# Optimization experiments

Measured on AMD Instinct MI355X. Metric: run time of the kernel, lower is better.

## Reference

```python
import jax, jax.numpy as jnp
import numpy as np

MAX_FREQ = 10
CORR_RADIUS = 2
PATCH = 9


def _gelu(x):
    return jax.nn.gelu(x, approximate=False)


def _project(coords, R, C0, f, pp):
    # coords [N,3] -> uv [ncams,N,2], cam-space z [ncams,N]
    d = coords[None, :, :] - C0[:, None, :]
    Xc = jnp.einsum('cij,cnj->cni', R, d)
    z = jnp.maximum(Xc[..., 2:3], 1e-6)
    uv = Xc[..., :2] / z * f[:, None, :] + pp[:, None, :]
    return uv, Xc[..., 2]


def _fourier(x, max_freq):
    freqs = (2.0 ** jnp.arange(max_freq, dtype=x.dtype)) * jnp.pi
    xf = x[..., None] * freqs
    enc = jnp.concatenate([jnp.sin(xf), jnp.cos(xf)], axis=-1)  # [...,D,2F]
    return enc.reshape(enc.shape[:-2] + (x.shape[-1] * 2 * max_freq,))


def _bilinear_time(img, t, gx, gy):
    # img [B,T,C,H,W]; t [B,K] int; gx,gy [B,K,P] normalized grid in [-1,1]
    # grid_sample(align_corners=False, padding_mode='zeros') via direct 4-tap gather
    B, T, C, H, W = img.shape
    x = (gx + 1.0) * 0.5 * W - 0.5
    y = (gy + 1.0) * 0.5 * H - 0.5
    x0 = jnp.floor(x)
    y0 = jnp.floor(y)
    wx = (x - x0)[..., None]
    wy = (y - y0)[..., None]
    x0 = x0.astype(jnp.int32)
    y0 = y0.astype(jnp.int32)
    b = jnp.arange(B)[:, None, None]
    tt = t[:, :, None]

    def tap(yy, xx):
        ok = ((xx >= 0) & (xx < W) & (yy >= 0) & (yy < H))[..., None]
        v = img[b, tt, :, jnp.clip(yy, 0, H - 1), jnp.clip(xx, 0, W - 1)]  # [B,K,P,C]
        return v * ok.astype(v.dtype)

    return (tap(y0, x0) * (1 - wx) * (1 - wy) + tap(y0, x0 + 1) * wx * (1 - wy)
            + tap(y0 + 1, x0) * (1 - wx) * wy + tap(y0 + 1, x0 + 1) * wx * wy)


def _conv2d(x, w, b):
    y = jax.lax.conv_general_dilated(x, w, (1, 1), 'SAME', dimension_numbers=('NCHW', 'OIHW', 'NCHW'))
    return y + b[None, :, None, None]


def _conv3d(x, w, b):
    y = jax.lax.conv_general_dilated(x, w, (1, 1, 1), 'SAME', dimension_numbers=('NCDHW', 'OIDHW', 'NCDHW'))
    return y + b[None, :, None, None, None]


def reference(views, cam_R, cam_center, cam_focal, cam_pp, query_coords, query_time, target_time, cube_scale, v2v_w, v2v_b, lin_vol_w, lin_vol_b, lin_pos_w, lin_pos_b, lin_depth_w, lin_depth_b, conv1_w, conv1_b, conv2_w, conv2_b, conv3_w, conv3_b, mlp1_w, mlp1_b, mlp2_w, mlp2_b, tq_emb, tt_emb, vis_emb_tab, depth_norm_scale, gate_w, gate_b, fus1_w, fus1_b, fus2_w, fus2_b):
    ncams, B, T, C, H, W = views.shape
    K = query_coords.shape[1]
    sizes = jnp.asarray([W, H], dtype=query_coords.dtype)

    # project query points to all cameras
    qflat = query_coords.reshape(-1, 3)
    p2d_flat, zc = _project(qflat, cam_R, cam_center, cam_focal, cam_pp)  # [ncams,BK,2]
    p2d_full = p2d_flat.reshape(ncams, B, K, 2)

    # fourier position embedding
    pp_n = jnp.transpose(p2d_full, (1, 2, 0, 3)) / sizes  # [B,K,ncams,2]
    embed_pos = _fourier(pp_n, MAX_FREQ) @ lin_pos_w.T + lin_pos_b

    # volume embedding: masked multi-camera cube sampling + 3D conv
    cs = 2 * CORR_RADIUS + 1
    P3 = cs ** 3
    row = (jnp.arange(cs, dtype=query_coords.dtype) - CORR_RADIUS) * (cube_scale * 2.0)
    gx3, gy3, gz3 = jnp.meshgrid(row, row, row, indexing='ij')
    xyz = jnp.stack([gx3, gy3, gz3], axis=-1).reshape(-1, 3)  # [P3,3], x outermost
    cube = (query_coords[:, :, None, :] + xyz).reshape(-1, 3)
    pc, _ = _project(cube, cam_R, cam_center, cam_focal, cam_pp)
    pc = pc.reshape(ncams, B, K, P3, 2)
    smps, msks = [], []
    for c in range(ncams):
        g = 2.0 * pc[c] / sizes - 1.0
        m = (g[..., 0] >= -1) & (g[..., 0] <= 1) & (g[..., 1] >= -1) & (g[..., 1] <= 1)
        s = _bilinear_time(views[c], query_time, g[..., 0], g[..., 1])  # [B,K,P3,C]
        smps.append(s)
        msks.append(m)
    vol = jnp.stack(smps)  # [ncams,B,K,P3,C]
    mf = jnp.stack(msks).astype(vol.dtype)[..., None]
    cnt = jnp.maximum(mf.sum(0), 1.0)
    mv = (vol * mf).sum(0) / cnt  # [B,K,P3,C]
    mv = mv.reshape(B, K, cs, cs, cs, C)  # (x,y,z,C)
    mv = jnp.transpose(mv, (0, 1, 5, 4, 3, 2)).reshape(B * K, C, cs, cs, cs)  # [(BK),C,z,y,x]
    mv = _gelu(_conv3d(mv, v2v_w, v2v_b))  # EmbedV2V: Conv3d(3,vdim,3) + GELU
    vd = mv.shape[1]
    mv = mv.reshape(B, K, vd, cs, cs, cs)
    mv = jnp.transpose(mv, (0, 1, 2, 5, 4, 3)).reshape(B, K, vd * P3)  # 'b t 1 (d total)'
    embed_volume = mv @ lin_vol_w.T + lin_vol_b
    embed_volume = jnp.broadcast_to(embed_volume[:, :, None, :], (B, K, ncams, embed_volume.shape[-1]))

    # patch embedding per camera
    lin = jnp.arange(PATCH, dtype=query_coords.dtype)
    gyy, gxx = jnp.meshgrid(lin, lin, indexing='ij')
    offs = jnp.stack([gxx - (PATCH - 1) / 2.0, gyy - (PATCH - 1) / 2.0], axis=-1)  # [P,P,2]
    pats = []
    for c in range(ncams):
        px = p2d_full[c][:, :, None, None, :] + offs  # [B,K,P,P,2]
        g = ((2.0 * px + 1.0) / sizes - 1.0).reshape(B, K, PATCH * PATCH, 2)
        s = _bilinear_time(views[c], query_time, g[..., 0], g[..., 1])  # [B,K,PP,C]
        pats.append(jnp.transpose(s.reshape(B, K, PATCH, PATCH, C), (0, 1, 4, 2, 3)))
    patches = jnp.stack(pats).reshape(ncams * B * K, C, PATCH, PATCH)
    x = _gelu(_conv2d(patches, conv1_w, conv1_b))
    x = _gelu(_conv2d(x, conv2_w, conv2_b))
    x = _gelu(_conv2d(x, conv3_w, conv3_b))
    x = x.reshape(x.shape[0], -1)  # 'b c p q -> b (c p q)'
    x = _gelu(x @ mlp1_w.T + mlp1_b)  # dropout is eval-mode identity
    emb_p = x @ mlp2_w.T + mlp2_b
    embed_patch = jnp.transpose(emb_p.reshape(ncams, B, K, -1), (1, 2, 0, 3))

    E = tq_emb.shape[1]
    embed_qt = jnp.broadcast_to(tq_emb[query_time][:, :, None, :], (B, K, ncams, E))
    embed_tt = jnp.broadcast_to(tt_emb[target_time][:, :, None, :], (B, K, ncams, E))

    # visibility (pinhole in-bounds check with margin=2)
    u = p2d_flat[..., 0]
    v = p2d_flat[..., 1]
    margin = 2.0
    vis = (zc > 0) & (u >= margin) & (u <= W - margin) & (v >= margin) & (v <= H - margin)
    vis = jnp.transpose(vis.reshape(ncams, B, K), (1, 2, 0))  # [B,K,ncams]
    embed_vis = vis_emb_tab[vis.astype(jnp.int32)]

    depths = jnp.linalg.norm(query_coords[:, :, None, :] - cam_center, axis=-1) / (cube_scale * depth_norm_scale[0])
    embed_depth = _fourier(depths[..., None], MAX_FREQ) @ lin_depth_w.T + lin_depth_b

    # gated fusion of 7 terms + fusion MLP
    terms = [embed_pos, embed_volume, embed_patch, embed_qt, embed_tt, embed_vis, embed_depth]
    gates = jax.nn.sigmoid(jnp.concatenate(terms, axis=-1) @ gate_w.T + gate_b)  # [B,K,ncams,7]
    fused = sum(gates[..., i:i + 1] * terms[i] for i in range(len(terms)))
    h = _gelu(fused @ fus1_w.T + fus1_b)
    embed_total = h @ fus2_w.T + fus2_b  # [B,K,ncams,decoder_dim]
    return embed_total, vis


def setup_inputs():
    ks = jax.random.split(jax.random.key(0), 24)
    ncams, B, T, C, H, W = 4, 2, 16, 3, 256, 256
    K, E, MF, cs, P, vdim = 256, 256, 10, 5, 9, 8
    views = jax.random.normal(ks[0], (ncams, B, T, C, H, W), jnp.float32)
    cam_R = jnp.tile(jnp.eye(3, dtype=jnp.float32)[None], (ncams, 1, 1))
    cam_center = jnp.stack([jnp.linspace(-0.5, 0.5, ncams), jnp.linspace(0.5, -0.5, ncams), jnp.full((ncams,), -5.0)], axis=-1).astype(jnp.float32)
    cam_focal = jnp.full((ncams, 2), 200.0, jnp.float32)
    cam_pp = jnp.full((ncams, 2), 128.0, jnp.float32)
    query_coords = jax.random.uniform(ks[1], (B, K, 3), jnp.float32, -1.0, 1.0)
    query_time = jax.random.randint(ks[2], (B, K), 0, T).astype(jnp.int32)
    target_time = jax.random.randint(ks[3], (B, K), 0, T).astype(jnp.int32)
    cube_scale = jnp.float32(0.02)

    def w(k, shape, s=0.02):
        return jax.random.normal(k, shape, jnp.float32) * s

    z = lambda n: jnp.zeros((n,), jnp.float32)
    return dict(
        views=views, cam_R=cam_R, cam_center=cam_center, cam_focal=cam_focal, cam_pp=cam_pp,
        query_coords=query_coords, query_time=query_time, target_time=target_time, cube_scale=cube_scale,
        v2v_w=w(ks[4], (vdim, C, 3, 3, 3)), v2v_b=z(vdim),
        lin_vol_w=w(ks[5], (E, cs ** 3 * vdim)), lin_vol_b=z(E),
        lin_pos_w=w(ks[6], (E, 4 * MF)), lin_pos_b=z(E),
        lin_depth_w=w(ks[7], (E, 2 * MF)), lin_depth_b=z(E),
        conv1_w=w(ks[8], (32, 3, 3, 3)), conv1_b=z(32),
        conv2_w=w(ks[9], (64, 32, 3, 3)), conv2_b=z(64),
        conv3_w=w(ks[10], (128, 64, 3, 3)), conv3_b=z(128),
        mlp1_w=w(ks[11], (2 * E, 128 * P * P)), mlp1_b=z(2 * E),
        mlp2_w=w(ks[12], (E, 2 * E)), mlp2_b=z(E),
        tq_emb=w(ks[13], (T, E), 1.0), tt_emb=w(ks[14], (T, E), 1.0),
        vis_emb_tab=w(ks[15], (2, E), 1.0),
        depth_norm_scale=jnp.array([500.0], jnp.float32),
        gate_w=w(ks[16], (7, 7 * E), 0.01), gate_b=z(7),
        fus1_w=w(ks[17], (4 * E, E)), fus1_b=z(4 * E),
        fus2_w=w(ks[18], (E, 4 * E)), fus2_b=z(E),
    )
```

## Files before the change

### kernel.cpp

```cpp
#include <hip/hip_runtime.h>
#include <hip/hip_bf16.h>

typedef __hip_bfloat16 bf16;
typedef __attribute__((ext_vector_type(8))) short short8;
typedef __attribute__((ext_vector_type(4))) float floatx4;

#define NC 4
#define BB 2
#define TS 16
#define CHN 3
#define HH 256
#define WW 256
#define KQ 256
#define EE 256
#define BKT 512
#define HW 65536
#define NSEG 25
#define CH1 32
#define CH1P 40
#define CH2 64
#define CH2P 72
#define PW 11

#define PB_WCL   32
#define PB_W23   160
#define PB_AUXW  416
#define PB_PROJ  424
#define PB_CUBE  936
#define PB_M1W   1448
#define PB_END   1452

__device__ __forceinline__ float tof(bf16 x){ return __bfloat162float(x); }
__device__ __forceinline__ bf16 tobf(float x){ return __float2bfloat16(x); }
__device__ __forceinline__ float gelu_f(float x){
    float t = fabsf(x) * 0.70710678118654752f;
    float k = __builtin_amdgcn_rcpf(fmaf(0.3275911f, t, 1.f));
    float p = fmaf(fmaf(fmaf(fmaf(1.061405429f, k, -1.453152027f), k,
                   1.421413741f), k, -0.284496736f), k, 0.254829592f) * k;
    float e = __expf(-t*t);
    float er = fmaf(-p, e, 1.f);
    float s = copysignf(er, x);
    return 0.5f*x*(1.f + s);
}
__device__ __forceinline__ float ldx(const void* p, size_t i, int bf){
    return bf ? tof(((const bf16*)p)[i]) : ((const float*)p)[i];
}
__device__ __forceinline__ void gload_lds16(const void* g, void* l){
    __builtin_amdgcn_global_load_lds((const __attribute__((address_space(1))) void*)g,
                                     (__attribute__((address_space(3))) void*)l, 16, 0, 0);
}
__device__ __forceinline__ unsigned pack2(float a, float b){
    union{ bf16 h[2]; unsigned u; } pk; pk.h[0]=tobf(a); pk.h[1]=tobf(b); return pk.u;
}

struct CvtArgs { const void* src[NSEG]; int dstoff[NSEG]; int cnt[NSEG]; };

struct PrepArgs {
    const void *camF, *camR, *camC, *camP, *qc, *csc;
    const void *c2w, *c3w, *linv, *f1w, *f2w, *m2w, *m1w, *views;
    const void *v2vw, *v2vb;
    const void *linpw, *lindw;
    const int* qtime;
    bf16 *w2cl, *w3cl, *linv_bf, *f1w_bf, *f2w_bf, *m2w_bf, *m1w_bf;
    float *p2d, *visf;
    float *linpwT, *lindwT;
    bf16* volf;
    void* dout;
    int* flagp;
};

union PrepSm {
    struct { float vol[3][7][7][7]; float ws[648]; float bs[8]; } cube;
    bf16 lin[10368];
};

__global__ __launch_bounds__(256) void prep_kernel(CvtArgs ca, float* __restrict__ pool, PrepArgs a)
{
    int bid = blockIdx.x, tid = threadIdx.x;
    int bf = (((const unsigned short*)a.camF)[0] != 0) ? 1 : 0;
    __shared__ PrepSm sm;

    if (bid < PB_WCL){
        for (int s=0; s<NSEG; ++s){
            const void* src = ca.src[s];
            float* d = pool + ca.dstoff[s];
            int n = ca.cnt[s];
            for (int i = bid*256 + tid; i < n; i += PB_WCL*256) d[i] = ldx(src, i, bf);
        }
    } else if (bid < PB_W23){
        int i0 = (bid-PB_WCL)*256 + tid;
        const int stride = (PB_W23-PB_WCL)*256;
        for (int i=i0; i<64*32*9; i+=stride){
            int oc=i/(32*9), r=i%(32*9), ic=r/9, tap=r%9;
            a.w2cl[tap*(64*CH1) + oc*CH1 + ic] = tobf(ldx(a.c2w, i, bf));
        }
        for (int i=i0; i<128*64*9; i+=stride){
            int oc=i/(64*9), r=i%(64*9), ic=r/9, tap=r%9;
            a.w3cl[tap*(128*CH2) + oc*CH2 + ic] = tobf(ldx(a.c3w, i, bf));
        }
    } else if (bid < PB_AUXW){
        int sub = (bid-PB_W23)>>6;
        int i0 = ((bid-PB_W23)&63)*256 + tid;
        const int stride = 64*256;
        if (sub==0){
            for (int i=i0; i<256*1024; i+=stride){
                int r=i>>10, c=i&1023;
                a.linv_bf[i] = tobf(c<1000 ? ldx(a.linv, (size_t)r*1000+c, bf) : 0.f);
            }
        } else if (sub==1){
            for (int i=i0; i<1024*256; i+=stride) a.f1w_bf[i]=tobf(ldx(a.f1w,i,bf));
        } else if (sub==2){
            for (int i=i0; i<256*1024; i+=stride) a.f2w_bf[i]=tobf(ldx(a.f2w,i,bf));
        } else {
            for (int i=i0; i<256*512; i+=stride) a.m2w_bf[i]=tobf(ldx(a.m2w,i,bf));
        }
    } else if (bid < PB_PROJ){
        if (bid==PB_AUXW && tid==0) *a.flagp = bf;
        int idx = (bid-PB_AUXW)*256 + tid;
        if (idx < NC*BKT){
            int c = idx / BKT, bk = idx % BKT;
            float dx = ldx(a.qc,bk*3+0,bf) - ldx(a.camC,c*3+0,bf);
            float dy = ldx(a.qc,bk*3+1,bf) - ldx(a.camC,c*3+1,bf);
            float dz = ldx(a.qc,bk*3+2,bf) - ldx(a.camC,c*3+2,bf);
            float X0 = ldx(a.camR,c*9+0,bf)*dx + ldx(a.camR,c*9+1,bf)*dy + ldx(a.camR,c*9+2,bf)*dz;
            float X1 = ldx(a.camR,c*9+3,bf)*dx + ldx(a.camR,c*9+4,bf)*dy + ldx(a.camR,c*9+5,bf)*dz;
            float X2 = ldx(a.camR,c*9+6,bf)*dx + ldx(a.camR,c*9+7,bf)*dy + ldx(a.camR,c*9+8,bf)*dz;
            float z = fmaxf(X2, 1e-6f);
            float u = X0/z*ldx(a.camF,c*2+0,bf) + ldx(a.camP,c*2+0,bf);
            float v = X1/z*ldx(a.camF,c*2+1,bf) + ldx(a.camP,c*2+1,bf);
            a.p2d[idx*2+0] = u; a.p2d[idx*2+1] = v;
            bool vis = (X2 > 0.f) && (u >= 2.f) && (u <= (float)WW-2.f) && (v >= 2.f) && (v <= (float)HH-2.f);
            a.visf[idx] = vis ? 1.f : 0.f;
            float vv = vis ? 1.f : 0.f;
            size_t vidx = (size_t)BB*KQ*NC*EE + (size_t)bk*NC + c;
            if (bf) ((bf16*)a.dout)[vidx] = tobf(vv);
            else    ((float*)a.dout)[vidx] = vv;
        }
    } else if (bid < PB_CUBE){
        int bk = bid - PB_PROJ;
        int c = tid & 3;
        int pg = tid >> 2;
        int b = bk >> 8;
        for (int i=tid; i<3*343; i+=256) ((float*)sm.cube.vol)[i]=0.f;
        for (int i=tid; i<648; i+=256) sm.cube.ws[i]=ldx(a.v2vw,i,bf);
        if (tid<8) sm.cube.bs[tid]=ldx(a.v2vb,tid,bf);
        __syncthreads();
        float cs2 = ldx(a.csc,0,bf) * 2.f;
        int t = a.qtime[bk];
        float qx0 = ldx(a.qc,bk*3+0,bf);
        float qy0 = ldx(a.qc,bk*3+1,bf);
        float qz0 = ldx(a.qc,bk*3+2,bf);
        float R0=ldx(a.camR,c*9+0,bf), R1=ldx(a.camR,c*9+1,bf), R2=ldx(a.camR,c*9+2,bf);
        float R3=ldx(a.camR,c*9+3,bf), R4=ldx(a.camR,c*9+4,bf), R5=ldx(a.camR,c*9+5,bf);
        float R6=ldx(a.camR,c*9+6,bf), R7=ldx(a.camR,c*9+7,bf), R8=ldx(a.camR,c*9+8,bf);
        float Cx=ldx(a.camC,c*3+0,bf), Cy=ldx(a.camC,c*3+1,bf), Cz=ldx(a.camC,c*3+2,bf);
        float Fx=ldx(a.camF,c*2+0,bf), Fy=ldx(a.camF,c*2+1,bf);
        float Px=ldx(a.camP,c*2+0,bf), Py=ldx(a.camP,c*2+1,bf);
        #pragma unroll
        for (int pass=0; pass<2; ++pass){
            int p = (pass<<6) + pg;
            bool act = p < 125;
            int i=p/25, j=(p/5)%5, kz=p%5;
            float a0=0.f,a1=0.f,a2=0.f,ms=0.f;
            if (act){
                float qx = qx0 + (float)(i-2)*cs2;
                float qy = qy0 + (float)(j-2)*cs2;
                float qz = qz0 + (float)(kz-2)*cs2;
                float dx=qx-Cx, dy=qy-Cy, dz=qz-Cz;
                float X0=R0*dx+R1*dy+R2*dz;
                float X1=R3*dx+R4*dy+R5*dz;
                float X2=R6*dx+R7*dy+R8*dz;
                float z = fmaxf(X2,1e-6f);
                float u = X0/z*Fx+Px, v = X1/z*Fy+Py;
                if (u>=0.f && u<=(float)WW && v>=0.f && v<=(float)HH){
                    ms = 1.f;
                    float x = u-0.5f, y = v-0.5f;
                    float xf = floorf(x), yf = floorf(y);
                    int ix=(int)xf, iy=(int)yf;
                    float wx=x-xf, wy=y-yf;
                    size_t basev = (size_t)((c*BB+b)*TS + t)*CHN*HW;
                    float wxs[2]={1.f-wx,wx}, wys[2]={1.f-wy,wy};
                    #pragma unroll
                    for (int ty=0;ty<2;++ty){
                        int yy=iy+ty; if (yy<0||yy>=HH) continue;
                        #pragma unroll
                        for (int tx=0;tx<2;++tx){
                            int xx=ix+tx; if (xx<0||xx>=WW) continue;
                            float wt=wys[ty]*wxs[tx];
                            size_t o = basev + (size_t)yy*WW+xx;
                            a0 += wt*ldx(a.views,o,bf);
                            a1 += wt*ldx(a.views,o+HW,bf);
                            a2 += wt*ldx(a.views,o+2*HW,bf);
                        }
                    }
                }
            }
            a0 += __shfl_xor(a0,1); a0 += __shfl_xor(a0,2);
            a1 += __shfl_xor(a1,1); a1 += __shfl_xor(a1,2);
            a2 += __shfl_xor(a2,1); a2 += __shfl_xor(a2,2);
            ms += __shfl_xor(ms,1); ms += __shfl_xor(ms,2);
            if (act && c==0){
                float cnt = fmaxf(ms,1.f);
                sm.cube.vol[0][kz+1][j+1][i+1]=a0/cnt;
                sm.cube.vol[1][kz+1][j+1][i+1]=a1/cnt;
                sm.cube.vol[2][kz+1][j+1][i+1]=a2/cnt;
            }
        }
        __syncthreads();
        if (tid >= 104 && tid < 128) a.volf[bk*1024 + 1000 + (tid-104)] = tobf(0.f);
        if (tid < 125){
            int w2=tid/25, h2=(tid/5)%5, d2=tid%5;
            for (int oc=0;oc<8;++oc){
                float acc = sm.cube.bs[oc];
                #pragma unroll
                for (int ic=0;ic<3;++ic)
                  #pragma unroll
                  for (int dz=0;dz<3;++dz)
                    #pragma unroll
                    for (int dy=0;dy<3;++dy)
                      #pragma unroll
                      for (int dxx=0;dxx<3;++dxx)
                        acc += sm.cube.vol[ic][d2+dz][h2+dy][w2+dxx] * sm.cube.ws[(((oc*3+ic)*3+dz)*3+dy)*3+dxx];
                a.volf[bk*1024 + oc*125 + tid] = tobf(gelu_f(acc));
            }
        }
    } else if (bid < PB_M1W){
        int n = bid - PB_CUBE;
        const size_t off = (size_t)n*10368;
        if (bf){
            const bf16* s = (const bf16*)a.m1w + off;
            for (int i=tid;i<10368;i+=256) sm.lin[i]=s[i];
        } else {
            const float* s = (const float*)a.m1w + off;
            for (int i=tid;i<10368;i+=256) sm.lin[i]=tobf(s[i]);
        }
        __syncthreads();
        unsigned* d = (unsigned*)(a.m1w_bf + off);
        for (int j2=tid; j2<5184; j2+=256){
            int j = j2*2;
            int pos0=j>>7, oc0=j&127;
            int pos1=(j+1)>>7, oc1=(j+1)&127;
            d[j2] = pack2(tof(sm.lin[oc0*81+pos0]), tof(sm.lin[oc1*81+pos1]));
        }
    } else {
        int i0 = (bid-PB_M1W)*256 + tid;
        for (int o=i0; o<10240; o+=1024){
            int j=o>>8, e=o&255;
            a.linpwT[o] = ldx(a.linpw, (size_t)e*40+j, bf);
        }
        for (int o=i0; o<5120; o+=1024){
            int j=o>>8, e=o&255;
            a.lindwT[o] = ldx(a.lindw, (size_t)e*20+j, bf);
        }
    }
}

struct __align__(16) PCShared {
    bf16 a2cl[11*PW*CH2P];
    bf16 a1cl[11*PW*CH1P];
    float w1s[864];
    float patch[3][11][11];
};
struct __align__(16) LVShared {
    bf16 As[64][72];
    bf16 Bs[64][72];
};

__device__ __forceinline__ void patchconv_body(
    PCShared& sm, int img,
    const void* __restrict__ views, const float* __restrict__ p2d,
    const int* __restrict__ qtime,
    const float* __restrict__ w1, const float* __restrict__ b1,
    const bf16* __restrict__ w2cl, const float* __restrict__ b2,
    const bf16* __restrict__ w3cl, const float* __restrict__ b3,
    bf16* __restrict__ act_out, const int* __restrict__ flagp)
{
    int c = img>>9, b = (img>>8)&1, k = img&255;
    int bk = b*KQ + k;
    int tid = threadIdx.x;
    int wave = tid>>6, lane = tid&63;

    for (int i=tid;i<3*11*11;i+=256) ((float*)sm.patch)[i]=0.f;
    for (int i=tid;i<864;i+=256) sm.w1s[i]=w1[i];
    {
        unsigned int* z1=(unsigned int*)sm.a1cl; int n1 = 11*PW*CH1P/2;
        for (int i=tid;i<n1;i+=256) z1[i]=0u;
        unsigned int* z2=(unsigned int*)sm.a2cl; int n2 = 11*PW*CH2P/2;
        for (int i=tid;i<n2;i+=256) z2[i]=0u;
    }
    __syncthreads();
    if (tid<243){
        int bf = *flagp;
        int ch = tid/81;
        int pp = tid - ch*81;
        float u=p2d[(c*BKT+bk)*2+0], v=p2d[(c*BKT+bk)*2+1];
        int t=qtime[bk];
        int r=pp/9,q=pp%9;
        float x=u+(float)(q-4), y=v+(float)(r-4);
        float xf=floorf(x), yf=floorf(y);
        int ix=(int)xf, iy=(int)yf;
        float wx=x-xf, wy=y-yf;
        size_t base = (size_t)((c*BB+b)*TS+t)*CHN*HW + (size_t)ch*HW;
        float acc=0.f;
        float wxs[2]={1.f-wx,wx}, wys[2]={1.f-wy,wy};
        #pragma unroll
        for (int ty=0;ty<2;++ty){
            int yy=iy+ty; if (yy<0||yy>=HH) continue;
            #pragma unroll
            for (int tx=0;tx<2;++tx){
                int xx=ix+tx; if (xx<0||xx>=WW) continue;
                acc += wys[ty]*wxs[tx]*ldx(views, base + (size_t)yy*WW+xx, bf);
            }
        }
        sm.patch[ch][r+1][q+1]=acc;
    }
    __syncthreads();
    for (int o=tid;o<81*32;o+=256){
        int oc=o&31, pp=o>>5;
// ... 96 lines not shown
                    *(uint2*)&outp[pos*128 + ocb] = pk;
                }
            }
        }
    }
}

__device__ __forceinline__ void linvol_body(
    LVShared& sm, int r, const bf16* __restrict__ A, const bf16* __restrict__ W,
    float* __restrict__ lvparts)
{
    int tid = threadIdx.x;
    int wave = tid>>6, lane = tid&63;
    int z = r>>5, rem = r&31, by = rem>>2, bx = rem&3;
    int m0 = by<<6, n0 = bx<<6;
    int kt0 = z*2;
    int lr = tid>>3, lc = (tid&7)<<3;
    floatx4 acc[4];
    #pragma unroll
    for (int j=0;j<4;++j) acc[j]=(floatx4){0.f,0.f,0.f,0.f};
    int arow = (wave<<4) + (lane&15);
    int koff = (lane>>4)<<3;
    int nrow = lane&15;
    for (int it=0; it<2; ++it){
        int ko = (kt0+it)<<6;
        *(uint4*)&sm.As[lr][lc]    = *(const uint4*)(A + (size_t)(m0+lr)*1024    + ko + lc);
        *(uint4*)&sm.As[lr+32][lc] = *(const uint4*)(A + (size_t)(m0+lr+32)*1024 + ko + lc);
        *(uint4*)&sm.Bs[lr][lc]    = *(const uint4*)(W + (size_t)(n0+lr)*1024    + ko + lc);
        *(uint4*)&sm.Bs[lr+32][lc] = *(const uint4*)(W + (size_t)(n0+lr+32)*1024 + ko + lc);
        __syncthreads();
        #pragma unroll
        for (int kk=0; kk<64; kk+=32){
            short8 af = *(const short8*)&sm.As[arow][kk+koff];
            #pragma unroll
            for (int j=0;j<4;++j){
                short8 wf = *(const short8*)&sm.Bs[(j<<4)+nrow][kk+koff];
                acc[j] = __builtin_amdgcn_mfma_f32_16x16x32_bf16(af, wf, acc[j], 0,0,0);
            }
        }
        __syncthreads();
    }
    float* out = lvparts + (size_t)z * (512*256);
    int crow = (wave<<4) + ((lane>>4)<<2);
    int ccol = lane&15;
    #pragma unroll
    for (int j=0;j<4;++j){
        int n = n0 + (j<<4) + ccol;
        #pragma unroll
        for (int rr=0;rr<4;++rr)
            out[(size_t)(m0+crow+rr)*256 + n] = acc[j][rr];
    }
}

__global__ __launch_bounds__(256) void patchlin_kernel(
    const void* __restrict__ views, const float* __restrict__ p2d,
    const int* __restrict__ qtime,
    const float* __restrict__ w1, const float* __restrict__ b1,
    const bf16* __restrict__ w2cl, const float* __restrict__ b2,
    const bf16* __restrict__ w3cl, const float* __restrict__ b3,
    bf16* __restrict__ act_out, int img0, int npc, const int* __restrict__ flagp,
    const bf16* __restrict__ volf, const bf16* __restrict__ linvw,
    float* __restrict__ lvparts)
{
    __shared__ union { PCShared pc; LVShared lv; } sm;
    int bid = blockIdx.x;
    if (bid < npc){
        patchconv_body(sm.pc, img0+bid, views, p2d, qtime, w1, b1, w2cl, b2, w3cl, b3,
                       act_out, flagp);
    } else {
        linvol_body(sm.lv, bid-npc, volf, linvw, lvparts);
    }
}

__global__ __launch_bounds__(256) void patchconv_kernel(
    const void* __restrict__ views, const float* __restrict__ p2d,
    const int* __restrict__ qtime,
    const float* __restrict__ w1, const float* __restrict__ b1,
    const bf16* __restrict__ w2cl, const float* __restrict__ b2,
    const bf16* __restrict__ w3cl, const float* __restrict__ b3,
    bf16* __restrict__ act_out, int img0, const int* __restrict__ flagp)
{
    __shared__ PCShared sm;
    patchconv_body(sm, img0+blockIdx.x, views, p2d, qtime, w1, b1, w2cl, b2, w3cl, b3,
                   act_out, flagp);
}

template<int OUT>
__global__ __launch_bounds__(256) void gemm_bf16_kernel(
    const bf16* __restrict__ A, const bf16* __restrict__ W, const float* __restrict__ bias,
    float* __restrict__ Cf, void* __restrict__ Cb, int M, int N, int K, int iters,
    int pstride)
{
    __shared__ bf16 As[2][64][72];
    __shared__ bf16 Bs[2][64][72];
    int tid = threadIdx.x;
    int wave = tid>>6, lane = tid&63;
    int m0 = blockIdx.y<<6, n0 = blockIdx.x<<6;
    int kt0 = blockIdx.z*iters;
    int lr = tid>>3;
    int lc = (tid&7)<<3;
    const bf16* Ap0 = A + (size_t)(m0+lr)*K    + (kt0<<6) + lc;
    const bf16* Ap1 = A + (size_t)(m0+lr+32)*K + (kt0<<6) + lc;
    const bf16* Wp0 = W + (size_t)(n0+lr)*K    + (kt0<<6) + lc;
    const bf16* Wp1 = W + (size_t)(n0+lr+32)*K + (kt0<<6) + lc;
    uint4 ra0 = *(const uint4*)Ap0;
    uint4 ra1 = *(const uint4*)Ap1;
    uint4 rb0 = *(const uint4*)Wp0;
    uint4 rb1 = *(const uint4*)Wp1;
    floatx4 acc[4];
    #pragma unroll
    for (int j=0;j<4;++j) acc[j] = (floatx4){0.f,0.f,0.f,0.f};
    int arow = (wave<<4) + (lane&15);
    int koff = (lane>>4)<<3;
    int nrow = lane&15;
    *(uint4*)&As[0][lr][lc]    = ra0;
    *(uint4*)&As[0][lr+32][lc] = ra1;
    *(uint4*)&Bs[0][lr][lc]    = rb0;
    *(uint4*)&Bs[0][lr+32][lc] = rb1;
    __syncthreads();
    for (int it=0; it<iters; ++it){
        int cur = it&1;
        if (it+1<iters){
            int off = (it+1)<<6;
            ra0 = *(const uint4*)(Ap0+off);
            ra1 = *(const uint4*)(Ap1+off);
            rb0 = *(const uint4*)(Wp0+off);
            rb1 = *(const uint4*)(Wp1+off);
        }
        #pragma unroll
        for (int kk=0; kk<64; kk+=32){
            short8 af = *(const short8*)&As[cur][arow][kk+koff];
            #pragma unroll
            for (int j=0;j<4;++j){
                short8 bfr = *(const short8*)&Bs[cur][(j<<4)+nrow][kk+koff];
                acc[j] = __builtin_amdgcn_mfma_f32_16x16x32_bf16(af, bfr, acc[j], 0, 0, 0);
            }
        }
        if (it+1<iters){
            __syncthreads();
            int nxt = cur^1;
            *(uint4*)&As[nxt][lr][lc]    = ra0;
            *(uint4*)&As[nxt][lr+32][lc] = ra1;
            *(uint4*)&Bs[nxt][lr][lc]    = rb0;
            *(uint4*)&Bs[nxt][lr+32][lc] = rb1;
            __syncthreads();
        }
    }
    int crow = (wave<<4) + ((lane>>4)<<2);
    int ccol = lane&15;
    #pragma unroll
    for (int j=0;j<4;++j){
        int n = n0 + (j<<4) + ccol;
        if (OUT==1){
            float bb = bias[n];
            #pragma unroll
            for (int r=0;r<4;++r)
                ((bf16*)Cb)[(size_t)(m0+crow+r)*N + n] = tobf(gelu_f(acc[j][r] + bb));
        } else {
            float* out = Cf + (size_t)blockIdx.z * pstride;
            #pragma unroll
            for (int r=0;r<4;++r)
                out[(size_t)(m0+crow+r)*N + n] = acc[j][r];
        }
    }
}

__global__ __launch_bounds__(256) void gemm128_kernel(
    const bf16* __restrict__ A, const bf16* __restrict__ W,
    float* __restrict__ Cf, int N, int K, int kiters_total, int zdiv, int pstride)
{
    __shared__ __align__(16) bf16 As[128][64];
    __shared__ __align__(16) bf16 Bs[128][64];
    int tid = threadIdx.x;
    int wave = tid>>6, lane = tid&63;
    int m0 = blockIdx.y<<7, n0 = blockIdx.x<<7;
    int it0 = (int)(((long)blockIdx.z     * kiters_total) / zdiv);
    int it1 = (int)(((long)(blockIdx.z+1) * kiters_total) / zdiv);
    float* out = Cf + (size_t)blockIdx.z * pstride;
    int srow = (wave<<5) + (lane>>3);
    int scol = (lane&7)<<3;
    const bf16* Ap = A + (size_t)(m0+srow)*K + ((size_t)it0<<6) + scol;
    const bf16* Bp = W + (size_t)(n0+srow)*K + ((size_t)it0<<6) + scol;
    bf16* AsW = &As[wave<<5][0];
    bf16* BsW = &Bs[wave<<5][0];
    floatx4 acc[4][4];
    #pragma unroll
    for (int i=0;i<4;++i)
      #pragma unroll
      for (int j=0;j<4;++j) acc[i][j] = (floatx4){0.f,0.f,0.f,0.f};
    int wm = (wave>>1)<<6, wn = (wave&1)<<6;
    int frow = lane&15, koff = (lane>>4)<<3;
    for (int it=it0; it<it1; ++it){
        size_t off = (size_t)(it-it0)<<6;
        #pragma unroll
        for (int j=0;j<4;++j){
            gload_lds16(Ap + (size_t)(j<<3)*K + off, AsW + (j<<3)*64);
            gload_lds16(Bp + (size_t)(j<<3)*K + off, BsW + (j<<3)*64);
        }
        __syncthreads();
        #pragma unroll
        for (int kk=0;kk<64;kk+=32){
            short8 af[4], bfv[4];
            #pragma unroll
            for (int i=0;i<4;++i) af[i]  = *(const short8*)&As[wm + (i<<4) + frow][kk+koff];
            #pragma unroll
            for (int j=0;j<4;++j) bfv[j] = *(const short8*)&Bs[wn + (j<<4) + frow][kk+koff];
            #pragma unroll
            for (int i=0;i<4;++i)
              #pragma unroll
              for (int j=0;j<4;++j)
                acc[i][j] = __builtin_amdgcn_mfma_f32_16x16x32_bf16(af[i], bfv[j], acc[i][j], 0,0,0);
        }
        __syncthreads();
    }
    int crow = (lane>>4)<<2;
    int ccol = lane&15;
    #pragma unroll
    for (int i=0;i<4;++i){
        int mrow = m0 + wm + (i<<4) + crow;
        #pragma unroll
        for (int j=0;j<4;++j){
            int n = n0 + wn + (j<<4) + ccol;
            #pragma unroll
            for (int r=0;r<4;++r)
                out[(size_t)(mrow+r)*N + n] = acc[i][j][r];
        }
    }
}

__global__ __launch_bounds__(256) void mlp1_fin_kernel(const float* __restrict__ P,
                                                       const float* __restrict__ bias,
                                                       bf16* __restrict__ Cb, int total, int Nmask,
                                                       int pstride){
    for (int i = blockIdx.x*256 + threadIdx.x; i < total; i += gridDim.x*256){
        float s = bias[i & Nmask];
        #pragma unroll
        for (int p=0;p<8;++p) s += P[(size_t)p*pstride + i];
        Cb[i] = tobf(gelu_f(s));
    }
}

__global__ __launch_bounds__(256) void fin2_kernel(const float* __restrict__ P,
                                                   const float* __restrict__ bias,
                                                   void* __restrict__ out, const int* __restrict__ flagp,
                                                   int total, int mask, int pstride){
    int bf = *flagp;
    for (int i = blockIdx.x*256 + threadIdx.x; i < total; i += gridDim.x*256){
        float s = bias[i & mask];
        #pragma unroll
        for (int p=0;p<4;++p) s += P[(size_t)p*pstride + i];
        if (bf) ((bf16*)out)[i] = tobf(s);
        else    ((float*)out)[i] = s;
    }
}

__global__ __launch_bounds__(256) void terms_kernel(
    const float* __restrict__ p2d, const float* __restrict__ visf,
    const float* __restrict__ lvp, const float* __restrict__ linv_b,
    const float* __restrict__ m2p, const float* __restrict__ m2_b,
    const float* __restrict__ linpwT, const float* __restrict__ lin_pos_b,
    const float* __restrict__ lindwT, const float* __restrict__ lin_depth_b,
    const float* __restrict__ tq_emb, const float* __restrict__ tt_emb,
    const float* __restrict__ vis_tab,
    const float* __restrict__ gate_w, const float* __restrict__ gate_b,
    const int* __restrict__ qtime, const int* __restrict__ ttime,
    const float* __restrict__ qc, const float* __restrict__ camC,
    const float* __restrict__ csc, const float* __restrict__ dns,
    bf16* __restrict__ fused)
{
    int row = blockIdx.x;
    int c = row & 3; int bk = row >> 2;
    int tid = threadIdx.x;
    __shared__ float feats[40];
    __shared__ float dfeat[20];
    __shared__ float terms[7][256];
    __shared__ float wred[4][7];
    __shared__ float gates_s[7];
    float u = p2d[(c*BKT+bk)*2+0], v = p2d[(c*BKT+bk)*2+1];
// ... 71 lines not shown
    const int*  qtime  = (const int*)d_in[6];
    const int*  ttime  = (const int*)d_in[7];

    char* base = (char*)d_ws;
    int*   flag = (int*)base;
    float* pool = (float*)(base + 256);

    CvtArgs ca; int poff = 0; int ns = 0;
    auto add = [&](const void* p, int n)->float* {
        ca.src[ns]=p; ca.dstoff[ns]=poff; ca.cnt[ns]=n;
        float* r = pool+poff; poff += n; ns++; return r;
    };
    float* P_camR = add(d_in[1],36);
    float* P_camC = add(d_in[2],12);
    float* P_camF = add(d_in[3],8);
    float* P_camP = add(d_in[4],8);
    float* P_qc   = add(d_in[5],1536);
    float* P_csc  = add(d_in[8],1);
    float* P_dns  = add(d_in[30],1);
    float* P_linvb= add(d_in[12],256);
    float* P_linpw= add(d_in[13],10240);
    float* P_linpb= add(d_in[14],256);
    float* P_lindw= add(d_in[15],5120);
    float* P_lindb= add(d_in[16],256);
    float* P_c1w  = add(d_in[17],864);
    float* P_c1b  = add(d_in[18],32);
    float* P_c2b  = add(d_in[20],64);
    float* P_c3b  = add(d_in[22],128);
    float* P_m1b  = add(d_in[24],512);
    float* P_m2b  = add(d_in[26],256);
    float* P_tq   = add(d_in[27],4096);
    float* P_tt   = add(d_in[28],4096);
    float* P_vtab = add(d_in[29],512);
    float* P_gw   = add(d_in[31],12544);
    float* P_gb   = add(d_in[32],7);
    float* P_f1b  = add(d_in[34],1024);
    float* P_f2b  = add(d_in[36],256);

    bf16* m1w_bf = (bf16*)(base + 4185600);
    bf16* w2cl   = (bf16*)(base + 14802432);
    bf16* w3cl   = (bf16*)(base + 14839296);
    bf16* linv_bf= (bf16*)(base + 14986752);
    bf16* f1w_bf = (bf16*)(base + 15511040);
    bf16* f2w_bf = (bf16*)(base + 16035328);
    bf16* m2w_bf = (bf16*)(base + 16559616);
    float* p2d   = (float*)(base + 16821760);
    float* visf  = (float*)(base + 16838144);
    bf16*  volf_bf = (bf16*)(base + 16846336);
    float* lvparts = (float*)(base + 17894912);
    float* linpwT  = (float*)(base + 22089216);
    float* lindwT  = (float*)(base + 22130176);
    bf16*  mlp1o_bf = (bf16*)(base + 24186368);
    bf16*  fusedb_bf= (bf16*)(base + 26283520);
    int NCH = (ws_size >= 103353856ull) ? 1 : 2;
    int MCH = 2048 / NCH;
    bf16*  c3act    = (bf16*)(base + 27332096);
    bf16*  hbuf_bf  = (bf16*)(base + 27332096);
    float* m2parts  = (float*)(base + 31526400);
    float* f2parts  = (float*)(base + 35720704);
    float* parts    = (float*)(base + 27332096 + (size_t)MCH*10368*2);

    PrepArgs pa;
    pa.camF=d_in[3]; pa.camR=d_in[1]; pa.camC=d_in[2]; pa.camP=d_in[4];
    pa.qc=d_in[5]; pa.csc=d_in[8];
    pa.c2w=d_in[19]; pa.c3w=d_in[21];
    pa.linv=d_in[11]; pa.f1w=d_in[33]; pa.f2w=d_in[35]; pa.m2w=d_in[25];
    pa.m1w=d_in[23]; pa.views=views;
    pa.v2vw=d_in[9]; pa.v2vb=d_in[10];
    pa.linpw=d_in[13]; pa.lindw=d_in[15];
    pa.qtime=qtime;
    pa.w2cl=w2cl; pa.w3cl=w3cl; pa.linv_bf=linv_bf; pa.f1w_bf=f1w_bf;
    pa.f2w_bf=f2w_bf; pa.m2w_bf=m2w_bf; pa.m1w_bf=m1w_bf;
    pa.p2d=p2d; pa.visf=visf; pa.volf=volf_bf;
    pa.linpwT=linpwT; pa.lindwT=lindwT;
    pa.dout=d_out; pa.flagp=flag;

    prep_kernel<<<PB_END, 256, 0, stream>>>(ca, pool, pa);

    if (NCH == 1){
        patchlin_kernel<<<2048+256, 256, 0, stream>>>(views, p2d, qtime, P_c1w, P_c1b,
                                                      w2cl, P_c2b, w3cl, P_c3b, c3act, 0, 2048, flag,
                                                      volf_bf, linv_bf, lvparts);
        gemm128_kernel<<<dim3(4, 16, 8), 256, 0, stream>>>(c3act, m1w_bf, parts,
                                                           512, 10368, 162, 8, 2048*512);
        mlp1_fin_kernel<<<512, 256, 0, stream>>>(parts, P_m1b, mlp1o_bf, 2048*512, 511, 2048*512);
    } else {
        gemm_bf16_kernel<2><<<dim3(4,8,8), 256, 0, stream>>>(volf_bf, linv_bf, nullptr, lvparts, nullptr,
                                                             512, 256, 1024, 2, 512*256);
        for (int ch=0; ch<NCH; ++ch){
            int img0 = ch*MCH;
            patchconv_kernel<<<MCH, 256, 0, stream>>>(views, p2d, qtime, P_c1w, P_c1b,
                                                      w2cl, P_c2b, w3cl, P_c3b, c3act, img0, flag);
            gemm128_kernel<<<dim3(4, MCH/128, 8), 256, 0, stream>>>(c3act, m1w_bf, parts,
                                                                    512, 10368, 162, 8, MCH*512);
            mlp1_fin_kernel<<<512, 256, 0, stream>>>(parts, P_m1b, mlp1o_bf + (size_t)img0*512,
                                                     MCH*512, 511, MCH*512);
        }
    }
    gemm_bf16_kernel<2><<<dim3(4,32,2), 256, 0, stream>>>(mlp1o_bf, m2w_bf, nullptr, m2parts, nullptr,
                                                          2048, 256, 512, 4, 2048*256);
    terms_kernel<<<2048, 256, 0, stream>>>(p2d, visf, lvparts, P_linvb, m2parts, P_m2b,
                                           linpwT, P_linpb, lindwT, P_lindb,
                                           P_tq, P_tt, P_vtab, P_gw, P_gb,
                                           qtime, ttime, P_qc, P_camC, P_csc, P_dns, fusedb_bf);
    gemm_bf16_kernel<1><<<dim3(16,32,1), 256, 0, stream>>>(fusedb_bf, f1w_bf, P_f1b, nullptr, hbuf_bf,
                                                           2048, 1024, 256, 4, 0);
    gemm_bf16_kernel<2><<<dim3(4,32,4), 256, 0, stream>>>(hbuf_bf, f2w_bf, nullptr, f2parts, nullptr,
                                                          2048, 256, 1024, 4, 2048*256);
    fin2_kernel<<<512, 256, 0, stream>>>(f2parts, P_f2b, d_out, flag, 2048*256, 255, 2048*256);
    (void)in_sizes; (void)n_in; (void)out_size;
}
```

Measured before the change: 377.4 us.

## Pipeline patch convolution with mlp1 GEMM across fused multi-role kernels

Splits the 2048 patch images into two halves and fuses kernels so that the mlp1 GEMM on the first half runs in the same launch as the patch convolution of the second half. Its final reduction runs alongside the GEMM of the second half. The mlp1 weight transpose and the auxiliary weight conversions move out of the prep kernel into the first patch-conv launch, so they overlap with convolution work. The goal is to fill idle compute units and hide the serial dependencies between conv, GEMM and reduction. In exchange it adds heterogeneous blocks with larger shared-memory unions, which may lower occupancy and depend on block scheduling order.

After: 416.3 us. +10.3%, slower.

```diff
diff --git a/kernel.cpp b/kernel.cpp
--- a/kernel.cpp
+++ b/kernel.cpp
@@ -22,13 +22,14 @@
 #define CH2P 72
 #define PW 11
 
-#define PB_WCL   32
-#define PB_W23   160
-#define PB_AUXW  416
-#define PB_PROJ  424
-#define PB_CUBE  936
-#define PB_M1W   1448
-#define PB_END   1452
+#define P_WCL   32
+#define P_W23   160
+#define P_LINV  224
+#define P_PROJ  232
+#define P_CUBE  744
+#define P_LPW   748
+#define P_M1WE  1260
+#define P_ENDF  1452
 
 __device__ __forceinline__ float tof(bf16 x){ return __bfloat162float(x); }
 __device__ __forceinline__ bf16 tobf(float x){ return __float2bfloat16(x); }
@@ -74,22 +75,54 @@
     bf16 lin[10368];
 };
 
+__device__ __forceinline__ void m1w_body(bf16* lin, int n, int tid,
+                                         const PrepArgs& a, int bf){
+    const size_t off = (size_t)n*10368;
+    if (bf){
+        const bf16* s = (const bf16*)a.m1w + off;
+        for (int i=tid;i<10368;i+=256) lin[i]=s[i];
+    } else {
+        const float* s = (const float*)a.m1w + off;
+        for (int i=tid;i<10368;i+=256) lin[i]=tobf(s[i]);
+    }
+    __syncthreads();
+    unsigned* d = (unsigned*)(a.m1w_bf + off);
+    for (int j2=tid; j2<5184; j2+=256){
+        int j = j2*2;
+        int pos0=j>>7, oc0=j&127;
+        int pos1=(j+1)>>7, oc1=(j+1)&127;
+        d[j2] = pack2(tof(lin[oc0*81+pos0]), tof(lin[oc1*81+pos1]));
+    }
+}
+__device__ __forceinline__ void aux3_body(int blk, int tid, const PrepArgs& a, int bf){
+    int sub = blk>>6;
+    int i0 = (blk&63)*256 + tid;
+    const int stride = 64*256;
+    if (sub==0){
+        for (int i=i0; i<1024*256; i+=stride) a.f1w_bf[i]=tobf(ldx(a.f1w,i,bf));
+    } else if (sub==1){
+        for (int i=i0; i<256*1024; i+=stride) a.f2w_bf[i]=tobf(ldx(a.f2w,i,bf));
+    } else {
+        for (int i=i0; i<256*512; i+=stride) a.m2w_bf[i]=tobf(ldx(a.m2w,i,bf));
+    }
+}
+
 __global__ __launch_bounds__(256) void prep_kernel(CvtArgs ca, float* __restrict__ pool, PrepArgs a)
 {
     int bid = blockIdx.x, tid = threadIdx.x;
     int bf = (((const unsigned short*)a.camF)[0] != 0) ? 1 : 0;
     __shared__ PrepSm sm;
 
-    if (bid < PB_WCL){
+    if (bid < P_WCL){
         for (int s=0; s<NSEG; ++s){
             const void* src = ca.src[s];
             float* d = pool + ca.dstoff[s];
             int n = ca.cnt[s];
-            for (int i = bid*256 + tid; i < n; i += PB_WCL*256) d[i] = ldx(src, i, bf);
-        }
-    } else if (bid < PB_W23){
-        int i0 = (bid-PB_WCL)*256 + tid;
-        const int stride = (PB_W23-PB_WCL)*256;
+            for (int i = bid*256 + tid; i < n; i += P_WCL*256) d[i] = ldx(src, i, bf);
+        }
+    } else if (bid < P_W23){
+        int i0 = (bid-P_WCL)*256 + tid;
+        const int stride = (P_W23-P_WCL)*256;
         for (int i=i0; i<64*32*9; i+=stride){
             int oc=i/(32*9), r=i%(32*9), ic=r/9, tap=r%9;
             a.w2cl[tap*(64*CH1) + oc*CH1 + ic] = tobf(ldx(a.c2w, i, bf));
@@ -98,25 +131,16 @@
             int oc=i/(64*9), r=i%(64*9), ic=r/9, tap=r%9;
             a.w3cl[tap*(128*CH2) + oc*CH2 + ic] = tobf(ldx(a.c3w, i, bf));
         }
-    } else if (bid < PB_AUXW){
-        int sub = (bid-PB_W23)>>6;
-        int i0 = ((bid-PB_W23)&63)*256 + tid;
+    } else if (bid < P_LINV){
+        int i0 = (bid-P_W23)*256 + tid;
         const int stride = 64*256;
-        if (sub==0){
-            for (int i=i0; i<256*1024; i+=stride){
-                int r=i>>10, c=i&1023;
-                a.linv_bf[i] = tobf(c<1000 ? ldx(a.linv, (size_t)r*1000+c, bf) : 0.f);
-            }
-        } else if (sub==1){
-            for (int i=i0; i<1024*256; i+=stride) a.f1w_bf[i]=tobf(ldx(a.f1w,i,bf));
-        } else if (sub==2){
-            for (int i=i0; i<256*1024; i+=stride) a.f2w_bf[i]=tobf(ldx(a.f2w,i,bf));
-        } else {
-            for (int i=i0; i<256*512; i+=stride) a.m2w_bf[i]=tobf(ldx(a.m2w,i,bf));
-        }
-    } else if (bid < PB_PROJ){
-        if (bid==PB_AUXW && tid==0) *a.flagp = bf;
-        int idx = (bid-PB_AUXW)*256 + tid;
+        for (int i=i0; i<256*1024; i+=stride){
+            int r=i>>10, c=i&1023;
+            a.linv_bf[i] = tobf(c<1000 ? ldx(a.linv, (size_t)r*1000+c, bf) : 0.f);
+        }
+    } else if (bid < P_PROJ){
+        if (bid==P_LINV && tid==0) *a.flagp = bf;
+        int idx = (bid-P_LINV)*256 + tid;
         if (idx < NC*BKT){
             int c = idx / BKT, bk = idx % BKT;
             float dx = ldx(a.qc,bk*3+0,bf) - ldx(a.camC,c*3+0,bf);
@@ -136,8 +160,8 @@
             if (bf) ((bf16*)a.dout)[vidx] = tobf(vv);
             else    ((float*)a.dout)[vidx] = vv;
         }
-    } else if (bid < PB_CUBE){
-        int bk = bid - PB_PROJ;
+    } else if (bid < P_CUBE){
+        int bk = bid - P_PROJ;
         int c = tid & 3;
         int pg = tid >> 2;
         int b = bk >> 8;
@@ -224,26 +248,8 @@
                 a.volf[bk*1024 + oc*125 + tid] = tobf(gelu_f(acc));
             }
         }
-    } else if (bid < PB_M1W){
-        int n = bid - PB_CUBE;
-        const size_t off = (size_t)n*10368;
-        if (bf){
-            const bf16* s = (const bf16*)a.m1w + off;
-            for (int i=tid;i<10368;i+=256) sm.lin[i]=s[i];
-        } else {
-            const float* s = (const float*)a.m1w + off;
-            for (int i=tid;i<10368;i+=256) sm.lin[i]=tobf(s[i]);
-        }
-        __syncthreads();
-        unsigned* d = (unsigned*)(a.m1w_bf + off);
-        for (int j2=tid; j2<5184; j2+=256){
-            int j = j2*2;
-            int pos0=j>>7, oc0=j&127;
-            int pos1=(j+1)>>7, oc1=(j+1)&127;
-            d[j2] = pack2(tof(sm.lin[oc0*81+pos0]), tof(sm.lin[oc1*81+pos1]));
-        }
-    } else {
-        int i0 = (bid-PB_M1W)*256 + tid;
+    } else if (bid < P_LPW){
+        int i0 = (bid-P_CUBE)*256 + tid;
         for (int o=i0; o<10240; o+=1024){
             int j=o>>8, e=o&255;
             a.linpwT[o] = ldx(a.linpw, (size_t)e*40+j, bf);
@@ -252,6 +258,10 @@
             int j=o>>8, e=o&255;
             a.lindwT[o] = ldx(a.lindw, (size_t)e*20+j, bf);
         }
+    } else if (bid < P_M1WE){
+        m1w_body(sm.lin, bid-P_LPW, tid, a, bf);
+    } else {
+        aux3_body(bid-P_M1WE, tid, a, bf);
     }
 }
 
@@ -264,6 +274,10 @@
 struct __align__(16) LVShared {
     bf16 As[64][72];
     bf16 Bs[64][72];
+};
+struct __align__(16) G128Shared {
+    bf16 As[128][64];
+    bf16 Bs[128][64];
 };
 
 __device__ __forceinline__ void patchconv_body(
@@ -466,23 +480,125 @@
     }
 }
 
-__global__ __launch_bounds__(256) void patchlin_kernel(
+__device__ __forceinline__ void gemm128_body(
+    G128Shared& s, int bid3, const bf16* __restrict__ A, const bf16* __restrict__ W,
+    float* __restrict__ Cf, int pstride)
+{
+    const int N=512, K=10368, kit=162, zdiv=8;
+    int tid = threadIdx.x;
+    int wave = tid>>6, lane = tid&63;
+    int m0 = ((bid3>>2)&7)<<7, n0 = (bid3&3)<<7;
+    int bz = bid3>>5;
+    int it0 = (int)(((long)bz     * kit) / zdiv);
+    int it1 = (int)(((long)(bz+1) * kit) / zdiv);
+    float* out = Cf + (size_t)bz * pstride;
+    int srow = (wave<<5) + (lane>>3);
+    int scol = (lane&7)<<3;
+    const bf16* Ap = A + (size_t)(m0+srow)*K + ((size_t)it0<<6) + scol;
+    const bf16* Bp = W + (size_t)(n0+srow)*K + ((size_t)it0<<6) + scol;
+    bf16* AsW = &s.As[wave<<5][0];
+    bf16* BsW = &s.Bs[wave<<5][0];
+    floatx4 acc[4][4];
+    #pragma unroll
+    for (int i=0;i<4;++i)
+      #pragma unroll
+      for (int j=0;j<4;++j) acc[i][j] = (floatx4){0.f,0.f,0.f,0.f};
+    int wm = (wave>>1)<<6, wn = (wave&1)<<6;
+    int frow = lane&15, koff = (lane>>4)<<3;
+    for (int it=it0; it<it1; ++it){
+        size_t off = (size_t)(it-it0)<<6;
+        #pragma unroll
+        for (int j=0;j<4;++j){
+            gload_lds16(Ap + (size_t)(j<<3)*K + off, AsW + (j<<3)*64);
+            gload_lds16(Bp + (size_t)(j<<3)*K + off, BsW + (j<<3)*64);
+        }
+        __syncthreads();
+        #pragma unroll
+        for (int kk=0;kk<64;kk+=32){
+            short8 af[4], bfv[4];
+            #pragma unroll
+            for (int i=0;i<4;++i) af[i]  = *(const short8*)&s.As[wm + (i<<4) + frow][kk+koff];
+            #pragma unroll
+            for (int j=0;j<4;++j) bfv[j] = *(const short8*)&s.Bs[wn + (j<<4) + frow][kk+koff];
+            #pragma unroll
+            for (int i=0;i<4;++i)
+              #pragma unroll
+              for (int j=0;j<4;++j)
+                acc[i][j] = __builtin_amdgcn_mfma_f32_16x16x32_bf16(af[i], bfv[j], acc[i][j], 0,0,0);
+        }
+        __syncthreads();
+    }
+    int crow = (lane>>4)<<2;
+    int ccol = lane&15;
+    #pragma unroll
+    for (int i=0;i<4;++i){
+        int mrow = m0 + wm + (i<<4) + crow;
+        #pragma unroll
+        for (int j=0;j<4;++j){
+            int n = n0 + wn + (j<<4) + ccol;
+            #pragma unroll
+            for (int r=0;r<4;++r)
+                out[(size_t)(mrow+r)*N + n] = acc[i][j][r];
+        }
+    }
+}
+
+__global__ __launch_bounds__(256) void patchlinA_kernel(
+    PrepArgs a, const float* __restrict__ w1, const float* __restrict__ b1,
+    const float* __restrict__ b2, const float* __restrict__ b3,
+    bf16* __restrict__ act_out, float* __restrict__ lvparts)
+{
+    __shared__ union { PCShared pc; LVShared lv; bf16 lin[10368]; } sm;
+    int bid = blockIdx.x, tid = threadIdx.x;
+    if (bid < 1024){
+        patchconv_body(sm.pc, bid, a.views, a.p2d, a.qtime, w1, b1, a.w2cl, b2, a.w3cl, b3,
+                       act_out, a.flagp);
+    } else if (bid < 1280){
+        linvol_body(sm.lv, bid-1024, a.volf, a.linv_bf, lvparts);
+    } else if (bid < 1792){
+        int bf = (((const unsigned short*)a.camF)[0] != 0) ? 1 : 0;
+        m1w_body(sm.lin, bid-1280, tid, a, bf);
+    } else {
+        int bf = (((const unsigned short*)a.camF)[0] != 0) ? 1 : 0;
+        aux3_body(bid-1792, tid, a, bf);
+    }
+}
+
+__global__ __launch_bounds__(256) void pc_g128_kernel(
     const void* __restrict__ views, const float* __restrict__ p2d,
     const int* __restrict__ qtime,
     const float* __restrict__ w1, const float* __restrict__ b1,
     const bf16* __restrict__ w2cl, const float* __restrict__ b2,
     const bf16* __restrict__ w3cl, const float* __restrict__ b3,
-    bf16* __restrict__ act_out, int img0, int npc, const int* __restrict__ flagp,
-    const bf16* __restrict__ volf, const bf16* __restrict__ linvw,
-    float* __restrict__ lvparts)
-{
-    __shared__ union { PCShared pc; LVShared lv; } sm;
+    bf16* __restrict__ act_out, const int* __restrict__ flagp,
+    const bf16* __restrict__ m1w_bf, float* __restrict__ partsA)
+{
+    __shared__ union { PCShared pc; G128Shared g; } sm;
     int bid = blockIdx.x;
-    if (bid < npc){
-        patchconv_body(sm.pc, img0+bid, views, p2d, qtime, w1, b1, w2cl, b2, w3cl, b3,
+    if (bid < 256){
+        gemm128_body(sm.g, bid, act_out, m1w_bf, partsA, 1024*512);
+    } else {
+        patchconv_body(sm.pc, 1024 + (bid-256), views, p2d, qtime, w1, b1, w2cl, b2, w3cl, b3,
                        act_out, flagp);
+    }
+}
+
+__global__ __launch_bounds__(256) void g128_fin_kernel(
+    const bf16* __restrict__ A1, const bf16* __restrict__ m1w_bf,
+    float* __restrict__ partsB, const float* __restrict__ partsA,
+    const float* __restrict__ m1b, bf16* __restrict__ out0)
+{
+    __shared__ G128Shared g;
+    int bid = blockIdx.x, tid = threadIdx.x;
+    if (bid < 256){
+        gemm128_body(g, bid, A1, m1w_bf, partsB, 1024*512);
     } else {
-        linvol_body(sm.lv, bid-npc, volf, linvw, lvparts);
+        for (int i=(bid-256)*256+tid; i<1024*512; i+=256*256){
+            float s = m1b[i & 511];
+            #pragma unroll
+            for (int p=0;p<8;++p) s += partsA[(size_t)p*(1024*512) + i];
+            out0[i] = tobf(gelu_f(s));
+        }
     }
 }
 
@@ -497,6 +613,68 @@
     __shared__ PCShared sm;
     patchconv_body(sm, img0+blockIdx.x, views, p2d, qtime, w1, b1, w2cl, b2, w3cl, b3,
                    act_out, flagp);
+}
+
+__global__ __launch_bounds__(256) void gemm128_kernel(
+    const bf16* __restrict__ A, const bf16* __restrict__ W,
+    float* __restrict__ Cf, int N, int K, int kiters_total, int zdiv, int pstride)
+{
+    __shared__ G128Shared s;
+    int tid = threadIdx.x;
+    int wave = tid>>6, lane = tid&63;
+    int m0 = blockIdx.y<<7, n0 = blockIdx.x<<7;
+    int it0 = (int)(((long)blockIdx.z     * kiters_total) / zdiv);
+    int it1 = (int)(((long)(blockIdx.z+1) * kiters_total) / zdiv);
+    float* out = Cf + (size_t)blockIdx.z * pstride;
+    int srow = (wave<<5) + (lane>>3);
+    int scol = (lane&7)<<3;
+    const bf16* Ap = A + (size_t)(m0+srow)*K + ((size_t)it0<<6) + scol;
+    const bf16* Bp = W + (size_t)(n0+srow)*K + ((size_t)it0<<6) + scol;
+    bf16* AsW = &s.As[wave<<5][0];
+    bf16* BsW = &s.Bs[wave<<5][0];
+    floatx4 acc[4][4];
+    #pragma unroll
+    for (int i=0;i<4;++i)
+      #pragma unroll
+      for (int j=0;j<4;++j) acc[i][j] = (floatx4){0.f,0.f,0.f,0.f};
+    int wm = (wave>>1)<<6, wn = (wave&1)<<6;
+    int frow = lane&15, koff = (lane>>4)<<3;
+    for (int it=it0; it<it1; ++it){
+        size_t off = (size_t)(it-it0)<<6;
+        #pragma unroll
+        for (int j=0;j<4;++j){
+            gload_lds16(Ap + (size_t)(j<<3)*K + off, AsW + (j<<3)*64);
+            gload_lds16(Bp + (size_t)(j<<3)*K + off, BsW + (j<<3)*64);
+        }
+        __syncthreads();
+        #pragma unroll
+        for (int kk=0;kk<64;kk+=32){
+            short8 af[4], bfv[4];
+            #pragma unroll
+            for (int i=0;i<4;++i) af[i]  = *(const short8*)&s.As[wm + (i<<4) + frow][kk+koff];
+            #pragma unroll
+            for (int j=0;j<4;++j) bfv[j] = *(const short8*)&s.Bs[wn + (j<<4) + frow][kk+koff];
+            #pragma unroll
+            for (int i=0;i<4;++i)
+              #pragma unroll
+              for (int j=0;j<4;++j)
+                acc[i][j] = __builtin_amdgcn_mfma_f32_16x16x32_bf16(af[i], bfv[j], acc[i][j], 0,0,0);
+        }
+        __syncthreads();
+    }
+    int crow = (lane>>4)<<2;
+    int ccol = lane&15;
+    #pragma unroll
+    for (int i=0;i<4;++i){
+        int mrow = m0 + wm + (i<<4) + crow;
+        #pragma unroll
+        for (int j=0;j<4;++j){
+            int n = n0 + wn + (j<<4) + ccol;
+            #pragma unroll
+            for (int r=0;r<4;++r)
+                out[(size_t)(mrow+r)*N + n] = acc[i][j][r];
+        }
+    }
 }
 
 template<int OUT>
@@ -575,69 +753,6 @@
             #pragma unroll
             for (int r=0;r<4;++r)
                 out[(size_t)(m0+crow+r)*N + n] = acc[j][r];
-        }
-    }
-}
-
-__global__ __launch_bounds__(256) void gemm128_kernel(
-    const bf16* __restrict__ A, const bf16* __restrict__ W,
-    float* __restrict__ Cf, int N, int K, int kiters_total, int zdiv, int pstride)
-{
-    __shared__ __align__(16) bf16 As[128][64];
-    __shared__ __align__(16) bf16 Bs[128][64];
-    int tid = threadIdx.x;
-    int wave = tid>>6, lane = tid&63;
-    int m0 = blockIdx.y<<7, n0 = blockIdx.x<<7;
-    int it0 = (int)(((long)blockIdx.z     * kiters_total) / zdiv);
-    int it1 = (int)(((long)(blockIdx.z+1) * kiters_total) / zdiv);
-    float* out = Cf + (size_t)blockIdx.z * pstride;
-    int srow = (wave<<5) + (lane>>3);
-    int scol = (lane&7)<<3;
-    const bf16* Ap = A + (size_t)(m0+srow)*K + ((size_t)it0<<6) + scol;
-    const bf16* Bp = W + (size_t)(n0+srow)*K + ((size_t)it0<<6) + scol;
-    bf16* AsW = &As[wave<<5][0];
-    bf16* BsW = &Bs[wave<<5][0];
-    floatx4 acc[4][4];
-    #pragma unroll
-    for (int i=0;i<4;++i)
-      #pragma unroll
-      for (int j=0;j<4;++j) acc[i][j] = (floatx4){0.f,0.f,0.f,0.f};
-    int wm = (wave>>1)<<6, wn = (wave&1)<<6;
-    int frow = lane&15, koff = (lane>>4)<<3;
-    for (int it=it0; it<it1; ++it){
-        size_t off = (size_t)(it-it0)<<6;
-        #pragma unroll
-        for (int j=0;j<4;++j){
-            gload_lds16(Ap + (size_t)(j<<3)*K + off, AsW + (j<<3)*64);
-            gload_lds16(Bp + (size_t)(j<<3)*K + off, BsW + (j<<3)*64);
-        }
-        __syncthreads();
-        #pragma unroll
-        for (int kk=0;kk<64;kk+=32){
-            short8 af[4], bfv[4];
-            #pragma unroll
-            for (int i=0;i<4;++i) af[i]  = *(const short8*)&As[wm + (i<<4) + frow][kk+koff];
-            #pragma unroll
-            for (int j=0;j<4;++j) bfv[j] = *(const short8*)&Bs[wn + (j<<4) + frow][kk+koff];
-            #pragma unroll
-            for (int i=0;i<4;++i)
-              #pragma unroll
-              for (int j=0;j<4;++j)
-                acc[i][j] = __builtin_amdgcn_mfma_f32_16x16x32_bf16(af[i], bfv[j], acc[i][j], 0,0,0);
-        }
-        __syncthreads();
-    }
-    int crow = (lane>>4)<<2;
-    int ccol = lane&15;
-    #pragma unroll
-    for (int i=0;i<4;++i){
-        int mrow = m0 + wm + (i<<4) + crow;
-        #pragma unroll
-        for (int j=0;j<4;++j){
-            int n = n0 + wn + (j<<4) + ccol;
-            #pragma unroll
-            for (int r=0;r<4;++r)
-                out[(size_t)(mrow+r)*N + n] = acc[i][j][r];
         }
     }
 }
@@ -815,13 +930,12 @@
     float* lindwT  = (float*)(base + 22130176);
     bf16*  mlp1o_bf = (bf16*)(base + 24186368);
     bf16*  fusedb_bf= (bf16*)(base + 26283520);
-    int NCH = (ws_size >= 103353856ull) ? 1 : 2;
-    int MCH = 2048 / NCH;
     bf16*  c3act    = (bf16*)(base + 27332096);
     bf16*  hbuf_bf  = (bf16*)(base + 27332096);
     float* m2parts  = (float*)(base + 31526400);
     float* f2parts  = (float*)(base + 35720704);
-    float* parts    = (float*)(base + 27332096 + (size_t)MCH*10368*2);
+    float* partsA   = (float*)(base + 69799424);
+    float* partsB   = (float*)(base + 86576640);
 
     PrepArgs pa;
     pa.camF=d_in[3]; pa.camR=d_in[1]; pa.camC=d_in[2]; pa.camP=d_in[4];
@@ -838,26 +952,33 @@
     pa.linpwT=linpwT; pa.lindwT=lindwT;
     pa.dout=d_out; pa.flagp=flag;
 
-    prep_kernel<<<PB_END, 256, 0, stream>>>(ca, pool, pa);
-
-    if (NCH == 1){
-        patchlin_kernel<<<2048+256, 256, 0, stream>>>(views, p2d, qtime, P_c1w, P_c1b,
-                                                      w2cl, P_c2b, w3cl, P_c3b, c3act, 0, 2048, flag,
-                                                      volf_bf, linv_bf, lvparts);
-        gemm128_kernel<<<dim3(4, 16, 8), 256, 0, stream>>>(c3act, m1w_bf, parts,
-                                                           512, 10368, 162, 8, 2048*512);
-        mlp1_fin_kernel<<<512, 256, 0, stream>>>(parts, P_m1b, mlp1o_bf, 2048*512, 511, 2048*512);
+    bool pipe = (ws_size >= 103353856ull);
+
+    if (pipe){
+        prep_kernel<<<P_LPW, 256, 0, stream>>>(ca, pool, pa);
+        patchlinA_kernel<<<1984, 256, 0, stream>>>(pa, P_c1w, P_c1b, P_c2b, P_c3b,
+                                                   c3act, lvparts);
+        pc_g128_kernel<<<1280, 256, 0, stream>>>(views, p2d, qtime, P_c1w, P_c1b,
+                                                 w2cl, P_c2b, w3cl, P_c3b, c3act, flag,
+                                                 m1w_bf, partsA);
+        g128_fin_kernel<<<512, 256, 0, stream>>>(c3act + (size_t)1024*10368, m1w_bf,
+                                                 partsB, partsA, P_m1b, mlp1o_bf);
+        mlp1_fin_kernel<<<512, 256, 0, stream>>>(partsB, P_m1b, mlp1o_bf + (size_t)1024*512,
+                                                 1024*512, 511, 1024*512);
     } else {
+        prep_kernel<<<P_ENDF, 256, 0, stream>>>(ca, pool, pa);
         gemm_bf16_kernel<2><<<dim3(4,8,8), 256, 0, stream>>>(volf_bf, linv_bf, nullptr, lvparts, nullptr,
                                                              512, 256, 1024, 2, 512*256);
-        for (int ch=0; ch<NCH; ++ch){
-            int img0 = ch*MCH;
-            patchconv_kernel<<<MCH, 256, 0, stream>>>(views, p2d, qtime, P_c1w, P_c1b,
-                                                      w2cl, P_c2b, w3cl, P_c3b, c3act, img0, flag);
-            gemm128_kernel<<<dim3(4, MCH/128, 8), 256, 0, stream>>>(c3act, m1w_bf, parts,
-                                                                    512, 10368, 162, 8, MCH*512);
-            mlp1_fin_kernel<<<512, 256, 0, stream>>>(parts, P_m1b, mlp1o_bf + (size_t)img0*512,
-                                                     MCH*512, 511, MCH*512);
+        bf16* c3act2 = (bf16*)(base + 27332096);
+        float* parts2 = (float*)(base + 27332096 + (size_t)1024*10368*2);
+        for (int ch=0; ch<2; ++ch){
+            int img0 = ch*1024;
+            patchconv_kernel<<<1024, 256, 0, stream>>>(views, p2d, qtime, P_c1w, P_c1b,
+                                                       w2cl, P_c2b, w3cl, P_c3b, c3act2, img0, flag);
+            gemm128_kernel<<<dim3(4, 8, 8), 256, 0, stream>>>(c3act2, m1w_bf, parts2,
+                                                              512, 10368, 162, 8, 1024*512);
+            mlp1_fin_kernel<<<512, 256, 0, stream>>>(parts2, P_m1b, mlp1o_bf + (size_t)img0*512,
+                                                     1024*512, 511, 1024*512);
         }
     }
     gemm_bf16_kernel<2><<<dim3(4,32,2), 256, 0, stream>>>(mlp1o_bf, m2w_bf, nullptr, m2parts, nullptr,
```
